# Optimization experiments

Measured on AMD Instinct MI355X. Metric: run time of the kernel, lower is better.

## Reference

```python
import jax, jax.numpy as jnp
import numpy as np

B, S, D_MODEL, H = 2, 2048, 512, 8
D_HEAD = D_MODEL // H  # 64; d_qk == d_model here


def setup_inputs() -> dict:
    key = jax.random.key(0)
    ks = jax.random.split(key, 7)
    sc = 1.0 / np.sqrt(D_MODEL)
    return {
        "x": jax.random.normal(ks[0], (B, S, D_MODEL), dtype=jnp.float32),
        "Wqk_w": jax.random.normal(ks[1], (2 * D_MODEL, D_MODEL), dtype=jnp.float32) * sc,
        "Wqk_b": jax.random.normal(ks[2], (2 * D_MODEL,), dtype=jnp.float32) * 0.01,
        "Wv_w": jax.random.normal(ks[3], (D_MODEL, D_MODEL), dtype=jnp.float32) * sc,
        "Wv_b": jax.random.normal(ks[4], (D_MODEL,), dtype=jnp.float32) * 0.01,
        "Wo_w": jax.random.normal(ks[5], (D_MODEL, D_MODEL), dtype=jnp.float32) * sc,
        "Wo_b": jax.random.normal(ks[6], (D_MODEL,), dtype=jnp.float32) * 0.01,
    }


def reference(x, Wqk_w, Wqk_b, Wv_w, Wv_b, Wo_w, Wo_b):
    b, s, _ = x.shape
    # projections
    qk = x @ Wqk_w.T + Wqk_b              # [B,S,2*d_qk]
    v = x @ Wv_w.T + Wv_b                 # [B,S,d_model]
    qk = qk.reshape(b, s, 2, H, D_HEAD)   # (two h d) layout
    v = v.reshape(b, s, H, D_HEAD)
    q, k = qk[:, :, 0], qk[:, :, 1]
    # generalized linear attention feature map: elu(x)+1
    q = jax.nn.elu(q) + 1.0
    k = jax.nn.elu(k) + 1.0
    scores = jnp.einsum('bthd,bshd->bhts', q, k)          # [B,H,T,S]
    mask = jnp.tril(jnp.ones((s, s), dtype=scores.dtype))  # causal multiplicative mask
    scores = scores * mask
    nu = scores.sum(axis=-1, keepdims=True)               # row normalizer
    attention = scores / nu
    context = jnp.einsum('bhts,bshd->bthd', attention, v)  # [B,T,H,D]
    out = context.reshape(b, s, D_MODEL) @ Wo_w.T + Wo_b
    return out
```

## Files before the change

kernel.cpp:

```cpp
#include <hip/hip_runtime.h>
#include <math.h>

#define B_N 2
#define S_N 2048
#define DM  512
#define H_N 8
#define DH  64
#define NC  32
#define CH  64

typedef __bf16 bf16x8 __attribute__((ext_vector_type(8)));
typedef float  f32x4  __attribute__((ext_vector_type(4)));

__device__ __forceinline__ unsigned short f2bf(float f) {
    unsigned int u = __float_as_uint(f);
    u += 0x7FFFu + ((u >> 16) & 1u);
    return (unsigned short)(u >> 16);
}

__device__ __forceinline__ void gload16(const void* g, void* l) {
    __builtin_amdgcn_global_load_lds(
        (const __attribute__((address_space(1))) unsigned int*)g,
        (__attribute__((address_space(3))) unsigned int*)l, 16, 0, 0);
}

__global__ __launch_bounds__(256) void convert_bf16(
    const float* __restrict__ x,  const float* __restrict__ wqk,
    const float* __restrict__ wv, const float* __restrict__ wo,
    unsigned short* __restrict__ xb,  unsigned short* __restrict__ wqkb,
    unsigned short* __restrict__ wvb, unsigned short* __restrict__ wob)
{
    int gid = blockIdx.x * 256 + threadIdx.x;
    const float* src; unsigned short* dst; int off;
    if (gid < 524288)      { src = x;   dst = xb;   off = gid; }
    else if (gid < 655360) { src = wqk; dst = wqkb; off = gid - 524288; }
    else if (gid < 720896) { src = wv;  dst = wvb;  off = gid - 655360; }
    else                   { src = wo;  dst = wob;  off = gid - 720896; }
    float4 v = ((const float4*)src)[off];
    ushort4 r; r.x = f2bf(v.x); r.y = f2bf(v.y); r.z = f2bf(v.z); r.w = f2bf(v.w);
    ((ushort4*)dst)[off] = r;
}

__global__ __launch_bounds__(256) void gemm_qkv_fused(
    const unsigned short* __restrict__ xb,
    const unsigned short* __restrict__ Wqkb,
    const unsigned short* __restrict__ Wvb,
    const float* __restrict__ bqk, const float* __restrict__ bv,
    unsigned short* __restrict__ qb, unsigned short* __restrict__ kb_,
    unsigned short* __restrict__ vtb,
    float* __restrict__ Asum, float* __restrict__ zsum)
{
    __shared__ unsigned short Alds[2 * 64 * 32];
    __shared__ unsigned short Blds[2 * 128 * 32];
    __shared__ unsigned short ktT[64 * 72];
    __shared__ unsigned short vtT[64 * 72];

    const int tid = threadIdx.x;
    const int w = tid >> 6, l = tid & 63;
    const int wm = w >> 1, wn = w & 1;
    const int lane15 = l & 15, quad = l >> 4;
    const int bx = blockIdx.x;
    const int m0 = blockIdx.y * 64;
    const int isq = (bx < 4);
    const int h = isq ? 0 : (bx - 4);

    const int srow = w * 16 + (l >> 2);
    const int skof = (l & 3) << 3;

    f32x4 acc[2][4];
    #pragma unroll
    for (int i = 0; i < 2; i++)
        #pragma unroll
        for (int j = 0; j < 4; j++) acc[i][j] = (f32x4){0.f, 0.f, 0.f, 0.f};

    for (int k0 = 0; k0 < DM; k0 += 64) {
        __syncthreads();
        gload16(&xb[(size_t)(m0 + srow) * DM + k0 + skof],      (char*)Alds + w * 1024);
        gload16(&xb[(size_t)(m0 + srow) * DM + k0 + 32 + skof], (char*)Alds + 4096 + w * 1024);
        if (isq) {
            gload16(&Wqkb[(size_t)(bx * 128 + srow) * DM + k0 + skof],           (char*)Blds + w * 1024);
            gload16(&Wqkb[(size_t)(bx * 128 + 64 + srow) * DM + k0 + skof],      (char*)Blds + 4096 + w * 1024);
            gload16(&Wqkb[(size_t)(bx * 128 + srow) * DM + k0 + 32 + skof],      (char*)Blds + 8192 + w * 1024);
            gload16(&Wqkb[(size_t)(bx * 128 + 64 + srow) * DM + k0 + 32 + skof], (char*)Blds + 12288 + w * 1024);
        } else {
            gload16(&Wqkb[(size_t)(512 + h * 64 + srow) * DM + k0 + skof],       (char*)Blds + w * 1024);
            gload16(&Wvb[(size_t)(h * 64 + srow) * DM + k0 + skof],              (char*)Blds + 4096 + w * 1024);
            gload16(&Wqkb[(size_t)(512 + h * 64 + srow) * DM + k0 + 32 + skof],  (char*)Blds + 8192 + w * 1024);
            gload16(&Wvb[(size_t)(h * 64 + srow) * DM + k0 + 32 + skof],         (char*)Blds + 12288 + w * 1024);
        }
        __syncthreads();

        #pragma unroll
        for (int s = 0; s < 2; s++) {
            bf16x8 af[2], bfr[4];
            #pragma unroll
            for (int i = 0; i < 2; i++)
                af[i] = *(bf16x8*)&Alds[s * 2048 + (wm * 32 + i * 16 + lane15) * 32 + quad * 8];
            #pragma unroll
            for (int j = 0; j < 4; j++)
                bfr[j] = *(bf16x8*)&Blds[s * 4096 + (wn * 64 + j * 16 + lane15) * 32 + quad * 8];
            #pragma unroll
            for (int i = 0; i < 2; i++)
                #pragma unroll
                for (int j = 0; j < 4; j++)
                    acc[i][j] = __builtin_amdgcn_mfma_f32_16x16x32_bf16(af[i], bfr[j], acc[i][j], 0, 0, 0);
        }
    }

    const int bbu = m0 >> 11;
    const int t0  = m0 & (S_N - 1);
    const int c0  = t0 >> 6;

    if (isq) {
        #pragma unroll
        for (int i = 0; i < 2; i++) {
            #pragma unroll
            for (int rg = 0; rg < 4; rg++) {
                int m = m0 + wm * 32 + i * 16 + quad * 4 + rg;
                int bb = m >> 11, t = m & (S_N - 1);
                #pragma unroll
                for (int j = 0; j < 4; j++) {
                    int n = bx * 128 + wn * 64 + j * 16 + lane15;
                    float val = acc[i][j][rg] + bqk[n];
                    val = (val > 0.f) ? (val + 1.f) : __expf(val);
                    qb[(((size_t)bb * H_N + (n >> 6)) * S_N + t) * DH + (n & 63)] = f2bf(val);
                }
            }
        }
        return;
    }

    #pragma unroll
    for (int i = 0; i < 2; i++) {
        #pragma unroll
        for (int rg = 0; rg < 4; rg++) {
            int tl = wm * 32 + i * 16 + quad * 4 + rg;
            int t  = t0 + tl;
            #pragma unroll
            for (int j = 0; j < 4; j++) {
                int col = j * 16 + lane15;
                if (wn == 0) {
                    float val = acc[i][j][rg] + bqk[512 + h * 64 + col];
                    val = (val > 0.f) ? (val + 1.f) : __expf(val);
                    unsigned short us = f2bf(val);
                    kb_[(((size_t)bbu * H_N + h) * S_N + t) * DH + col] = us;
                    ktT[col * 72 + tl] = us;
                } else {
                    float val = acc[i][j][rg] + bv[h * 64 + col];
                    vtT[col * 72 + tl] = f2bf(val);
                }
            }
        }
    }
    __syncthreads();

    {
        size_t vbase = (((size_t)bbu * H_N + h) * DH) * S_N + t0;
        #pragma unroll
        for (int it = 0; it < 2; it++) {
            int idx = it * 2048 + tid * 8;
            int d = idx >> 6, tt = idx & 63;
            *(bf16x8*)&vtb[vbase + (size_t)d * S_N + tt] = *(bf16x8*)&vtT[d * 72 + tt];
        }
    }

    {
        int blk = ((bbu * H_N + h) * NC) + c0;
        bf16x8 va[2];
        #pragma unroll
        for (int s = 0; s < 2; s++)
            va[s] = *(bf16x8*)&vtT[(w * 16 + lane15) * 72 + s * 32 + quad * 8];
        f32x4 sacc[4];
        #pragma unroll
        for (int j = 0; j < 4; j++) sacc[j] = (f32x4){0.f, 0.f, 0.f, 0.f};
        #pragma unroll
        for (int j = 0; j < 4; j++)
            #pragma unroll
            for (int s = 0; s < 2; s++) {
                bf16x8 kB = *(bf16x8*)&ktT[(j * 16 + lane15) * 72 + s * 32 + quad * 8];
                sacc[j] = __builtin_amdgcn_mfma_f32_16x16x32_bf16(va[s], kB, sacc[j], 0, 0, 0);
            }
        #pragma unroll
        for (int j = 0; j < 4; j++)
            #pragma unroll
            for (int rg = 0; rg < 4; rg++)
                Asum[(size_t)blk * 4096 + (w * 16 + quad * 4 + rg) * 64 + j * 16 + lane15] = sacc[j][rg];
    }

    if (tid < 64) {
        float z = 0.f;
        #pragma unroll
        for (int p = 0; p < 8; p++) {
            bf16x8 kk = *(bf16x8*)&ktT[tid * 72 + p * 8];
            #pragma unroll
            for (int e = 0; e < 8; e++) z += (float)kk[e];
        }
        zsum[(size_t)((bbu * H_N + h) * NC + c0) * 64 + tid] = z;
    }
}

__global__ __launch_bounds__(256) void attn_mfma(
    const unsigned short* __restrict__ qb, const unsigned short* __restrict__ kb_,
    const unsigned short* __restrict__ vtb, const float* __restrict__ Asum,
    const float* __restrict__ zsum, unsigned short* __restrict__ ctxb)
{
    __shared__ __align__(16) unsigned short P[64 * 72];
    __shared__ __align__(16) unsigned short Spre[64 * 72];
    __shared__ float nupart[64][4];
    __shared__ float zc_s[64];

    const int bid = blockIdx.x;
    const int xcd = bid & 7, idx = bid >> 3;
    const int bh = xcd + 8 * (idx & 1);
    const int c  = idx >> 1;
    const int b = bh >> 3, h = bh & 7;
    const int tid = threadIdx.x;
    const int w = tid >> 6, l = tid & 63;
    const int lane15 = l & 15, quad = l >> 4;

    const unsigned short* qc  = qb  + (size_t)bh * S_N * DH + c * CH * DH;
    const unsigned short* kc  = kb_ + (size_t)bh * S_N * DH + c * CH * DH;
    const unsigned short* vtc = vtb + (size_t)bh * DH * S_N + c * CH;

    {
        const float* abase = Asum + (size_t)bh * NC * 4096;
        const int e = tid * 16;
        float4 a0 = {0,0,0,0}, a1 = {0,0,0,0}, a2 = {0,0,0,0}, a3 = {0,0,0,0};
        for (int cc = 0; cc < c; cc++) {
            const float4* p = (const float4*)(abase + (size_t)cc * 4096 + e);
            float4 p0 = p[0], p1 = p[1], p2 = p[2], p3 = p[3];
            a0.x += p0.x; a0.y += p0.y; a0.z += p0.z; a0.w += p0.w;
            a1.x += p1.x; a1.y += p1.y; a1.z += p1.z; a1.w += p1.w;
            a2.x += p2.x; a2.y += p2.y; a2.z += p2.z; a2.w += p2.w;
            a3.x += p3.x; a3.y += p3.y; a3.z += p3.z; a3.w += p3.w;
        }
        const int d2 = e >> 6, d1 = e & 63;
        ushort4 u0 = {f2bf(a0.x), f2bf(a0.y), f2bf(a0.z), f2bf(a0.w)};
        ushort4 u1 = {f2bf(a1.x), f2bf(a1.y), f2bf(a1.z), f2bf(a1.w)};
        ushort4 u2 = {f2bf(a2.x), f2bf(a2.y), f2bf(a2.z), f2bf(a2.w)};
        ushort4 u3 = {f2bf(a3.x), f2bf(a3.y), f2bf(a3.z), f2bf(a3.w)};
        *(ushort4*)&Spre[d2 * 72 + d1]      = u0;
        *(ushort4*)&Spre[d2 * 72 + d1 + 4]  = u1;
        *(ushort4*)&Spre[d2 * 72 + d1 + 8]  = u2;
        *(ushort4*)&Spre[d2 * 72 + d1 + 12] = u3;

        if (tid < 64) {
            const float* zbase = zsum + (size_t)bh * NC * 64 + tid;
            float z = 0.f;
            for (int cc = 0; cc < c; cc++) z += zbase[cc * 64];
            zc_s[tid] = z;
        }
    }

    bf16x8 af[2];
    #pragma unroll
    for (int s = 0; s < 2; s++)
        af[s] = *(const bf16x8*)&qc[(w * 16 + lane15) * DH + s * 32 + quad * 8];

    f32x4 sacc[4];
    #pragma unroll
    for (int j = 0; j < 4; j++) sacc[j] = (f32x4){0.f, 0.f, 0.f, 0.f};
    #pragma unroll
    for (int j = 0; j < 4; j++)
        #pragma unroll
        for (int s = 0; s < 2; s++) {
            bf16x8 bk = *(const bf16x8*)&kc[(j * 16 + lane15) * DH + s * 32 + quad * 8];
            sacc[j] = __builtin_amdgcn_mfma_f32_16x16x32_bf16(af[s], bk, sacc[j], 0, 0, 0);
        }

    const int r0 = w * 16 + quad * 4;
    #pragma unroll
    for (int j = 0; j < 4; j++) {
        int u = j * 16 + lane15;
        #pragma unroll
        for (int rg = 0; rg < 4; rg++) {
            int rr = r0 + rg;
            float v = (u <= rr) ? sacc[j][rg] : 0.f;
            P[rr * 72 + u] = f2bf(v);
        }
    }
    __syncthreads();

    const int tl = tid >> 2, part = tid & 3;
    float nup = 0.f;
    {
        bf16x8 p0 = *(const bf16x8*)&P[tl * 72 + part * 16];
        bf16x8 p1 = *(const bf16x8*)&P[tl * 72 + part * 16 + 8];
        bf16x8 q0 = *(const bf16x8*)&qc[tl * DH + part * 16];
        bf16x8 q1 = *(const bf16x8*)&qc[tl * DH + part * 16 + 8];
        #pragma unroll
        for (int i = 0; i < 8; i++) {
            nup += (float)p0[i] + (float)p1[i];
            nup += (float)q0[i] * zc_s[part * 16 + i];
            nup += (float)q1[i] * zc_s[part * 16 + 8 + i];
        }
    }
    nupart[tl][part] = nup;
    __syncthreads();

    bf16x8 pa[2];
    #pragma unroll
    for (int s = 0; s < 2; s++)
        pa[s] = *(const bf16x8*)&P[(w * 16 + lane15) * 72 + s * 32 + quad * 8];

    f32x4 acc[4];
    #pragma unroll
    for (int j = 0; j < 4; j++) acc[j] = (f32x4){0.f, 0.f, 0.f, 0.f};
    #pragma unroll
    for (int j = 0; j < 4; j++)
        #pragma unroll
        for (int s = 0; s < 2; s++) {
            bf16x8 bv8 = *(const bf16x8*)&vtc[(size_t)(j * 16 + lane15) * S_N + s * 32 + quad * 8];
            acc[j] = __builtin_amdgcn_mfma_f32_16x16x32_bf16(pa[s], bv8, acc[j], 0, 0, 0);
            bf16x8 bs = *(const bf16x8*)&Spre[(j * 16 + lane15) * 72 + s * 32 + quad * 8];
            acc[j] = __builtin_amdgcn_mfma_f32_16x16x32_bf16(af[s], bs, acc[j], 0, 0, 0);
        }

    #pragma unroll
    for (int rg = 0; rg < 4; rg++) {
        int rr = r0 + rg;
        float nu = nupart[rr][0] + nupart[rr][1] + nupart[rr][2] + nupart[rr][3];
        float inv = 1.f / nu;
        size_t obase = ((size_t)b * S_N + c * CH + rr) * DM + h * DH;
        #pragma unroll
        for (int j = 0; j < 4; j++)
            ctxb[obase + j * 16 + lane15] = f2bf(acc[j][rg] * inv);
    }
}

__global__ __launch_bounds__(256) void gemm_out_mfma(
    const unsigned short* __restrict__ ctxb,
    const unsigned short* __restrict__ Wob,
    const float* __restrict__ bo, float* __restrict__ out)
{
    __shared__ unsigned short Alds[2 * 64 * 32];
    __shared__ unsigned short Blds[2 * 64 * 32];
    const int tid = threadIdx.x;
    const int w = tid >> 6, l = tid & 63;
    const int wm = w >> 1, wn = w & 1;
    const int lane15 = l & 15, quad = l >> 4;
    const int n0 = blockIdx.x * 64;
    const int m0 = blockIdx.y * 64;

    const int srow = w * 16 + (l >> 2);
    const int skof = (l & 3) << 3;

    f32x4 acc[2][2];
    #pragma unroll
    for (int i = 0; i < 2; i++)
        #pragma unroll
        for (int j = 0; j < 2; j++) acc[i][j] = (f32x4){0.f, 0.f, 0.f, 0.f};

    for (int k0 = 0; k0 < DM; k0 += 64) {
        __syncthreads();
        gload16(&ctxb[(size_t)(m0 + srow) * DM + k0 + skof],      (char*)Alds + w * 1024);
        gload16(&ctxb[(size_t)(m0 + srow) * DM + k0 + 32 + skof], (char*)Alds + 4096 + w * 1024);
        gload16(&Wob[(size_t)(n0 + srow) * DM + k0 + skof],       (char*)Blds + w * 1024);
        gload16(&Wob[(size_t)(n0 + srow) * DM + k0 + 32 + skof],  (char*)Blds + 4096 + w * 1024);
        __syncthreads();

        #pragma unroll
        for (int s = 0; s < 2; s++) {
            bf16x8 af2[2], bfr[2];
            #pragma unroll
            for (int i = 0; i < 2; i++)
                af2[i] = *(bf16x8*)&Alds[s * 2048 + (wm * 32 + i * 16 + lane15) * 32 + quad * 8];
            #pragma unroll
            for (int j = 0; j < 2; j++)
                bfr[j] = *(bf16x8*)&Blds[s * 2048 + (wn * 32 + j * 16 + lane15) * 32 + quad * 8];
            #pragma unroll
            for (int i = 0; i < 2; i++)
                #pragma unroll
                for (int j = 0; j < 2; j++)
                    acc[i][j] = __builtin_amdgcn_mfma_f32_16x16x32_bf16(af2[i], bfr[j], acc[i][j], 0, 0, 0);
        }
    }

    #pragma unroll
    for (int i = 0; i < 2; i++) {
        #pragma unroll
        for (int rg = 0; rg < 4; rg++) {
            int m = m0 + wm * 32 + i * 16 + quad * 4 + rg;
            #pragma unroll
            for (int j = 0; j < 2; j++) {
                int n = n0 + wn * 32 + j * 16 + lane15;
                out[(size_t)m * DM + n] = acc[i][j][rg] + bo[n];
            }
        }
    }
}

extern "C" void kernel_launch(void* const* d_in, const int* in_sizes, int n_in,
                              void* d_out, int out_size, void* d_ws, size_t ws_size,
                              hipStream_t stream)
{
    const float* x   = (const float*)d_in[0];
    const float* Wqk = (const float*)d_in[1];
    const float* bqk = (const float*)d_in[2];
    const float* Wv  = (const float*)d_in[3];
    const float* bv  = (const float*)d_in[4];
    const float* Wo  = (const float*)d_in[5];
    const float* bo  = (const float*)d_in[6];
    float* out = (float*)d_out;

    const size_t NTOK = (size_t)B_N * S_N * DM;
    float* Asum = (float*)d_ws;
    float* zsum = Asum + NTOK;
    unsigned short* xb   = (unsigned short*)(zsum + 32768);
    unsigned short* Wqkb = xb   + NTOK;
    unsigned short* Wvb  = Wqkb + 524288;
    unsigned short* Wob  = Wvb  + 262144;
    unsigned short* qb   = Wob  + 262144;
    unsigned short* kb_  = qb   + NTOK;
    unsigned short* vtb  = kb_  + NTOK;
    unsigned short* ctxb = vtb  + NTOK;

    convert_bf16  <<<dim3(3072),   256, 0, stream>>>(x, Wqk, Wv, Wo, xb, Wqkb, Wvb, Wob);
    gemm_qkv_fused<<<dim3(12, 64), 256, 0, stream>>>(xb, Wqkb, Wvb, bqk, bv, qb, kb_, vtb, Asum, zsum);
    attn_mfma     <<<dim3(512),    256, 0, stream>>>(qb, kb_, vtb, Asum, zsum, ctxb);
    gemm_out_mfma <<<dim3(8, 64),  256, 0, stream>>>(ctxb, Wob, bo, out);
}
```

Baseline: 121.2 us.

## Compute chunk prefix sums once via last-block atomic counter in QKV GEMM

Replaces the per-chunk redundant prefix summation of KV state and k-sums in the attention kernel (each block summed up to 31 previous chunks) with a single exclusive scan. The last QKV GEMM block to finish for each batch-head, detected with an atomic counter reset in the convert kernel, performs the scan. It writes bf16 prefix states to a new workspace buffer and overwrites zsum in place. The attention kernel then reads its precomputed prefix directly from global memory instead of LDS. This trades quadratic redundant reads for a serialized tail in 16 blocks plus extra fences and atomics, and it drops the XCD-aware block mapping.

```diff
diff --git a/kernel.cpp b/kernel.cpp
--- a/kernel.cpp
+++ b/kernel.cpp
@@ -28,9 +28,12 @@
     const float* __restrict__ x,  const float* __restrict__ wqk,
     const float* __restrict__ wv, const float* __restrict__ wo,
     unsigned short* __restrict__ xb,  unsigned short* __restrict__ wqkb,
-    unsigned short* __restrict__ wvb, unsigned short* __restrict__ wob)
+    unsigned short* __restrict__ wvb, unsigned short* __restrict__ wob,
+    unsigned* __restrict__ cnt)
 {
     int gid = blockIdx.x * 256 + threadIdx.x;
+    if (blockIdx.x == 0 && threadIdx.x < 16)
+        __hip_atomic_store(&cnt[threadIdx.x], 0u, __ATOMIC_RELAXED, __HIP_MEMORY_SCOPE_AGENT);
     const float* src; unsigned short* dst; int off;
     if (gid < 524288)      { src = x;   dst = xb;   off = gid; }
     else if (gid < 655360) { src = wqk; dst = wqkb; off = gid - 524288; }
@@ -48,12 +51,14 @@
     const float* __restrict__ bqk, const float* __restrict__ bv,
     unsigned short* __restrict__ qb, unsigned short* __restrict__ kb_,
     unsigned short* __restrict__ vtb,
-    float* __restrict__ Asum, float* __restrict__ zsum)
+    float* __restrict__ Asum, float* __restrict__ zsum,
+    unsigned short* __restrict__ Sptb, unsigned* __restrict__ cnt)
 {
     __shared__ unsigned short Alds[2 * 64 * 32];
     __shared__ unsigned short Blds[2 * 128 * 32];
     __shared__ unsigned short ktT[64 * 72];
     __shared__ unsigned short vtT[64 * 72];
+    __shared__ int lastflag;
 
     const int tid = threadIdx.x;
     const int w = tid >> 6, l = tid & 63;
@@ -197,22 +202,68 @@
         }
         zsum[(size_t)((bbu * H_N + h) * NC + c0) * 64 + tid] = z;
     }
+
+    __threadfence();
+    __syncthreads();
+    if (tid == 0) {
+        unsigned old = __hip_atomic_fetch_add(&cnt[bbu * H_N + h], 1u,
+                          __ATOMIC_ACQ_REL, __HIP_MEMORY_SCOPE_AGENT);
+        lastflag = (old == NC - 1);
+    }
+    __syncthreads();
+    if (!lastflag) return;
+    __threadfence();
+
+    {
+        const int bh = bbu * H_N + h;
+        const float* abase = Asum + (size_t)bh * NC * 4096;
+        unsigned short* sbase = Sptb + (size_t)bh * NC * 4096;
+        const int e = tid * 16;
+        float4 a0 = {0,0,0,0}, a1 = {0,0,0,0}, a2 = {0,0,0,0}, a3 = {0,0,0,0};
+        #pragma unroll 4
+        for (int cc = 0; cc < NC; cc++) {
+            const float4* p = (const float4*)(abase + (size_t)cc * 4096 + e);
+            float4 p0 = p[0], p1 = p[1], p2 = p[2], p3 = p[3];
+            ushort4 u0 = {f2bf(a0.x), f2bf(a0.y), f2bf(a0.z), f2bf(a0.w)};
+            ushort4 u1 = {f2bf(a1.x), f2bf(a1.y), f2bf(a1.z), f2bf(a1.w)};
+            ushort4 u2 = {f2bf(a2.x), f2bf(a2.y), f2bf(a2.z), f2bf(a2.w)};
+            ushort4 u3 = {f2bf(a3.x), f2bf(a3.y), f2bf(a3.z), f2bf(a3.w)};
+            unsigned short* sp = sbase + (size_t)cc * 4096 + e;
+            *(ushort4*)(sp)      = u0;
+            *(ushort4*)(sp + 4)  = u1;
+            *(ushort4*)(sp + 8)  = u2;
+            *(ushort4*)(sp + 12) = u3;
+            a0.x += p0.x; a0.y += p0.y; a0.z += p0.z; a0.w += p0.w;
+            a1.x += p1.x; a1.y += p1.y; a1.z += p1.z; a1.w += p1.w;
+            a2.x += p2.x; a2.y += p2.y; a2.z += p2.z; a2.w += p2.w;
+            a3.x += p3.x; a3.y += p3.y; a3.z += p3.z; a3.w += p3.w;
+        }
+        if (tid < 64) {
+            size_t zb = (size_t)bh * NC * 64 + tid;
+            float vals[NC];
+            #pragma unroll
+            for (int cc = 0; cc < NC; cc++) vals[cc] = zsum[zb + cc * 64];
+            float zacc = 0.f;
+            #pragma unroll
+            for (int cc = 0; cc < NC; cc++) {
+                float tmp = vals[cc];
+                zsum[zb + cc * 64] = zacc;
+                zacc += tmp;
+            }
+        }
+    }
 }
 
 __global__ __launch_bounds__(256) void attn_mfma(
     const unsigned short* __restrict__ qb, const unsigned short* __restrict__ kb_,
-    const unsigned short* __restrict__ vtb, const float* __restrict__ Asum,
+    const unsigned short* __restrict__ vtb, const unsigned short* __restrict__ Sptb,
     const float* __restrict__ zsum, unsigned short* __restrict__ ctxb)
 {
     __shared__ __align__(16) unsigned short P[64 * 72];
-    __shared__ __align__(16) unsigned short Spre[64 * 72];
     __shared__ float nupart[64][4];
-    __shared__ float zc_s[64];
-
-    const int bid = blockIdx.x;
-    const int xcd = bid & 7, idx = bid >> 3;
-    const int bh = xcd + 8 * (idx & 1);
-    const int c  = idx >> 1;
+
+    const int blk = blockIdx.x;
+    const int bh = blk >> 5, c = blk & 31;
     const int b = bh >> 3, h = bh & 7;
     const int tid = threadIdx.x;
     const int w = tid >> 6, l = tid & 63;
@@ -221,36 +272,8 @@
     const unsigned short* qc  = qb  + (size_t)bh * S_N * DH + c * CH * DH;
     const unsigned short* kc  = kb_ + (size_t)bh * S_N * DH + c * CH * DH;
     const unsigned short* vtc = vtb + (size_t)bh * DH * S_N + c * CH;
-
-    {
-        const float* abase = Asum + (size_t)bh * NC * 4096;
-        const int e = tid * 16;
-        float4 a0 = {0,0,0,0}, a1 = {0,0,0,0}, a2 = {0,0,0,0}, a3 = {0,0,0,0};
-        for (int cc = 0; cc < c; cc++) {
-            const float4* p = (const float4*)(abase + (size_t)cc * 4096 + e);
-            float4 p0 = p[0], p1 = p[1], p2 = p[2], p3 = p[3];
-            a0.x += p0.x; a0.y += p0.y; a0.z += p0.z; a0.w += p0.w;
-            a1.x += p1.x; a1.y += p1.y; a1.z += p1.z; a1.w += p1.w;
-            a2.x += p2.x; a2.y += p2.y; a2.z += p2.z; a2.w += p2.w;
-            a3.x += p3.x; a3.y += p3.y; a3.z += p3.z; a3.w += p3.w;
-        }
-        const int d2 = e >> 6, d1 = e & 63;
-        ushort4 u0 = {f2bf(a0.x), f2bf(a0.y), f2bf(a0.z), f2bf(a0.w)};
-        ushort4 u1 = {f2bf(a1.x), f2bf(a1.y), f2bf(a1.z), f2bf(a1.w)};
-        ushort4 u2 = {f2bf(a2.x), f2bf(a2.y), f2bf(a2.z), f2bf(a2.w)};
-        ushort4 u3 = {f2bf(a3.x), f2bf(a3.y), f2bf(a3.z), f2bf(a3.w)};
-        *(ushort4*)&Spre[d2 * 72 + d1]      = u0;
-        *(ushort4*)&Spre[d2 * 72 + d1 + 4]  = u1;
-        *(ushort4*)&Spre[d2 * 72 + d1 + 8]  = u2;
-        *(ushort4*)&Spre[d2 * 72 + d1 + 12] = u3;
-
-        if (tid < 64) {
-            const float* zbase = zsum + (size_t)bh * NC * 64 + tid;
-            float z = 0.f;
-            for (int cc = 0; cc < c; cc++) z += zbase[cc * 64];
-            zc_s[tid] = z;
-        }
-    }
+    const unsigned short* spc = Sptb + (size_t)blk * 4096;
+    const float* zc = zsum + (size_t)blk * 64;
 
     bf16x8 af[2];
     #pragma unroll
@@ -291,8 +314,8 @@
         #pragma unroll
         for (int i = 0; i < 8; i++) {
             nup += (float)p0[i] + (float)p1[i];
-            nup += (float)q0[i] * zc_s[part * 16 + i];
-            nup += (float)q1[i] * zc_s[part * 16 + 8 + i];
+            nup += (float)q0[i] * zc[part * 16 + i];
+            nup += (float)q1[i] * zc[part * 16 + 8 + i];
         }
     }
     nupart[tl][part] = nup;
@@ -312,7 +335,7 @@
         for (int s = 0; s < 2; s++) {
             bf16x8 bv8 = *(const bf16x8*)&vtc[(size_t)(j * 16 + lane15) * S_N + s * 32 + quad * 8];
             acc[j] = __builtin_amdgcn_mfma_f32_16x16x32_bf16(pa[s], bv8, acc[j], 0, 0, 0);
-            bf16x8 bs = *(const bf16x8*)&Spre[(j * 16 + lane15) * 72 + s * 32 + quad * 8];
+            bf16x8 bs = *(const bf16x8*)&spc[(j * 16 + lane15) * 64 + s * 32 + quad * 8];
             acc[j] = __builtin_amdgcn_mfma_f32_16x16x32_bf16(af[s], bs, acc[j], 0, 0, 0);
         }
 
@@ -413,10 +436,13 @@
     unsigned short* qb   = Wob  + 262144;
     unsigned short* kb_  = qb   + NTOK;
     unsigned short* vtb  = kb_  + NTOK;
-    unsigned short* ctxb = vtb  + NTOK;
-
-    convert_bf16  <<<dim3(3072),   256, 0, stream>>>(x, Wqk, Wv, Wo, xb, Wqkb, Wvb, Wob);
-    gemm_qkv_fused<<<dim3(12, 64), 256, 0, stream>>>(xb, Wqkb, Wvb, bqk, bv, qb, kb_, vtb, Asum, zsum);
-    attn_mfma     <<<dim3(512),    256, 0, stream>>>(qb, kb_, vtb, Asum, zsum, ctxb);
+    unsigned short* Sptb = vtb  + NTOK;
+    unsigned short* ctxb = Sptb + NTOK;
+    unsigned* cnt        = (unsigned*)(ctxb + NTOK);
+
+    convert_bf16  <<<dim3(3072),   256, 0, stream>>>(x, Wqk, Wv, Wo, xb, Wqkb, Wvb, Wob, cnt);
+    gemm_qkv_fused<<<dim3(12, 64), 256, 0, stream>>>(xb, Wqkb, Wvb, bqk, bv, qb, kb_, vtb,
+                                                     Asum, zsum, Sptb, cnt);
+    attn_mfma     <<<dim3(512),    256, 0, stream>>>(qb, kb_, vtb, Sptb, zsum, ctxb);
     gemm_out_mfma <<<dim3(8, 64),  256, 0, stream>>>(ctxb, Wob, bo, out);
 }
```

New measurement: 220.9 us. 1.82x slower.
